# Performance work log

Hardware: AMD Instinct MI355X
Metric: run time of the kernel (lower is better)

The kernel has to match this reference:

```python
import jax, jax.numpy as jnp
import numpy as np
from jax import lax

B_J0 = 0.01      # baseline threshold b_j0
BETA = 1.8       # adaptation strength (isAdapt=1)
GAMMA = 0.5      # surrogate-gradient scale
LENS = 0.5       # surrogate-gradient window
TAU_M = 20.0     # membrane time constant
DT = 1.0
HID = 800
OUT = 10
IN = 28
DECODE = 50

@jax.custom_vjp
def act_fun(x):
    # Heaviside spike with rectangular surrogate gradient
    return (x > 0).astype(x.dtype)

def _act_fwd(x):
    return act_fun(x), x

def _act_bwd(x, g):
    return (GAMMA * g * (jnp.abs(x) < LENS).astype(g.dtype),)

act_fun.defvjp(_act_fwd, _act_bwd)

def setup_inputs() -> dict:
    key = jax.random.key(0)
    ks = jax.random.split(key, 8)
    N = 2048
    x = jax.random.normal(ks[0], (N, 784), jnp.float32)
    # xavier-ish init for i2h / h2o, orthogonal-ish scale for h2h
    W_i2h = jax.random.normal(ks[1], (HID, IN), jnp.float32) * (1.0 / np.sqrt(IN))
    b_i2h = jnp.zeros((HID,), jnp.float32)
    W_h2h = jax.random.normal(ks[2], (HID, HID), jnp.float32) * (1.0 / np.sqrt(HID))
    b_h2h = jnp.zeros((HID,), jnp.float32)
    W_h2o = jax.random.normal(ks[3], (OUT, HID), jnp.float32) * (1.0 / np.sqrt(HID))
    b_h2o = jax.random.normal(ks[4], (OUT,), jnp.float32) * 0.01
    tau_adp_h = jnp.full((HID,), 700.0, jnp.float32)
    tau_adp_o = jnp.full((OUT,), 700.0, jnp.float32)
    return {"x": x, "W_i2h": W_i2h, "b_i2h": b_i2h, "W_h2h": W_h2h,
            "b_h2h": b_h2h, "W_h2o": W_h2o, "b_h2o": b_h2o,
            "tau_adp_h": tau_adp_h, "tau_adp_o": tau_adp_o}

def reference(x, W_i2h, b_i2h, W_h2h, b_h2h, W_h2o, b_h2o, tau_adp_h, tau_adp_o):
    N = x.shape[0]
    T = 784 // IN  # 28 encode steps
    # [N, 784] -> [N, IN, T] -> pad 50 zero decode steps -> time-major [T+50, N, IN]
    seq = x.reshape(N, IN, T)
    seq = jnp.concatenate([seq, jnp.zeros((N, IN, DECODE), seq.dtype)], axis=2)
    seq = jnp.transpose(seq, (2, 0, 1))
    alpha = jnp.exp(-DT / jnp.asarray(TAU_M, x.dtype))
    ro_h = jnp.exp(-DT / tau_adp_h)  # [HID]
    ro_o = jnp.exp(-DT / tau_adp_o)  # [OUT]
    mask = (jnp.arange(T + DECODE) >= T).astype(x.dtype)  # accumulate only decode steps

    def step(carry, inp):
        h_mem, h_spk, b_h, o_mem, o_spk, b_o, acc = carry
        xt, m = inp
        # hidden adaptive-LIF update (mem_update_NU_adp)
        h_in = xt @ W_i2h.T + b_i2h + h_spk @ W_h2h.T + b_h2h
        b_h = ro_h * b_h + (1.0 - ro_h) * h_spk
        Bh = B_J0 + BETA * b_h
        h_mem = h_mem * alpha + (1.0 - alpha) * h_in - Bh * h_spk * DT
        h_spk = act_fun(h_mem - Bh)
        # output adaptive-LIF update (mem_update_adp with h2o)
        o_in = h_spk @ W_h2o.T + b_h2o
        b_o = ro_o * b_o + (1.0 - ro_o) * o_spk
        Bo = B_J0 + BETA * b_o
        o_mem = o_mem * alpha + (1.0 - alpha) * o_in - Bo * o_spk * DT
        o_spk = act_fun(o_mem - Bo)
        acc = acc + m * o_spk
        return (h_mem, h_spk, b_h, o_mem, o_spk, b_o, acc), None

    carry0 = (jnp.zeros((N, HID), x.dtype), jnp.zeros((N, HID), x.dtype),
              jnp.full((N, HID), B_J0, x.dtype),
              jnp.zeros((N, OUT), x.dtype), jnp.zeros((N, OUT), x.dtype),
              jnp.full((N, OUT), B_J0, x.dtype),
              jnp.zeros((N, OUT), x.dtype))
    final, _ = lax.scan(step, carry0, (seq, mask))
    return final[6]
```

## Files before the change

### kernel.cpp

```cpp
#include <hip/hip_runtime.h>
#include <math.h>
#include <stdint.h>

namespace {
constexpr int N_    = 2048;
constexpr int H_    = 800;
constexpr int IN_   = 28;
constexpr int TENC  = 28;
constexpr int TTOT  = 78;
constexpr int ONUM  = 10;
constexpr int PODS  = 8;
constexpr int PBLK  = 26;
constexpr int NBLK  = PODS * PBLK;
constexpr int NTILE = 26;
constexpr int FSTR  = 32;
constexpr int NSEG  = 13 * 4 * 2;
constexpr int SMEM_B = NSEG * 1024;
constexpr int SMEM_W = IN_ * 32 * 4;
constexpr int AROW  = 27;
constexpr int SMEM_A = 8 * 32 * AROW * 4;
constexpr int SMEM_TOT = SMEM_B + SMEM_W + SMEM_A;
}

typedef __attribute__((ext_vector_type(4))) int v4i;

__device__ __forceinline__ void digitize(float w, int8_t d[4]) {
    double dd = (double)w * 4294967296.0;
    long long r = (long long)rint(dd);
    int8_t d0 = (int8_t)(r & 255); r = (r - (long long)d0) >> 8;
    int8_t d1 = (int8_t)(r & 255); r = (r - (long long)d1) >> 8;
    int8_t d2 = (int8_t)(r & 255); r = (r - (long long)d2) >> 8;
    long long r3 = r; r3 = r3 > 127 ? 127 : (r3 < -128 ? -128 : r3);
    d[0] = d0; d[1] = d1; d[2] = d2; d[3] = (int8_t)r3;
}

__device__ __forceinline__ v4i unpack16(uint32_t u) {
    v4i f;
    f[0] = (int)((((u      ) & 0xFu) * 0x00204081u) & 0x01010101u);
    f[1] = (int)((((u >>  4) & 0xFu) * 0x00204081u) & 0x01010101u);
    f[2] = (int)((((u >>  8) & 0xFu) * 0x00204081u) & 0x01010101u);
    f[3] = (int)((((u >> 12) & 0xFu) * 0x00204081u) & 0x01010101u);
    return f;
}

__device__ __forceinline__ void pod_barrier(uint32_t* __restrict__ flags,
                                            int pod, int l, uint32_t epoch) {
    __syncthreads();
    if (threadIdx.x < 64) {
        if (threadIdx.x == 0) {
            asm volatile("s_waitcnt vmcnt(0)" ::: "memory");
            __hip_atomic_store(flags + pod * FSTR + l, epoch,
                               __ATOMIC_RELAXED, __HIP_MEMORY_SCOPE_AGENT);
        }
        const bool mine = (threadIdx.x < PBLK);
        bool done = false;
        while (!done) {
            bool ok = true;
            if (mine)
                ok = (__hip_atomic_load(flags + pod * FSTR + threadIdx.x,
                        __ATOMIC_RELAXED, __HIP_MEMORY_SCOPE_AGENT) >= epoch);
            done = (__ballot(ok) == ~0ull);
            if (!done) __builtin_amdgcn_s_sleep(1);
        }
    }
    __syncthreads();
}

__global__ void prep_kernel(const float* __restrict__ x, float* __restrict__ xt2,
                            uint32_t* __restrict__ sp0, uint32_t* __restrict__ sp1,
                            uint32_t* __restrict__ flags)
{
    size_t idx = (size_t)blockIdx.x * blockDim.x + threadIdx.x;
    size_t stride = (size_t)gridDim.x * blockDim.x;
    const size_t TOT = (size_t)TENC * N_ * IN_;
    for (size_t e = idx; e < TOT; e += stride) {
        int t = (int)(e / (N_ * IN_));
        int rem = (int)(e % (N_ * IN_));
        int n = rem / IN_, c = rem % IN_;
        xt2[e] = x[(size_t)n * 784 + c * TENC + t];
    }
    const size_t PW = (size_t)NTILE * N_;
    for (size_t e = idx; e < PW; e += stride) { sp0[e] = 0u; sp1[e] = 0u; }
    for (size_t e = idx; e < (size_t)PODS * FSTR; e += stride) flags[e] = 0u;
}

__global__ __launch_bounds__(512)
__attribute__((amdgpu_waves_per_eu(2)))
void lsnn_persist(const float* __restrict__ xt2,
                  const float* __restrict__ Wi,
                  const float* __restrict__ b_i2h,
                  const float* __restrict__ Wh,
                  const float* __restrict__ b_h2h,
                  const float* __restrict__ Wo,
                  const float* __restrict__ b_h2o,
                  const float* __restrict__ tau_h,
                  const float* __restrict__ tau_o,
                  uint32_t* sp0, uint32_t* sp1,
                  uint32_t* flags,
                  float* __restrict__ out)
{
    extern __shared__ __align__(16) int8_t smem[];
    int8_t*   Bl  = smem;
    float*    wl  = (float*)(smem + SMEM_B);
    uint32_t* Alds = (uint32_t*)(smem + SMEM_B + SMEM_W);

    const int bid  = blockIdx.x;
    const int pod  = bid / PBLK;
    const int l    = bid % PBLK;
    const bool is_o = (l == 25);
    const int it   = is_o ? 0 : l;
    const int i0   = it * 32;
    const int wv   = threadIdx.x >> 6;
    const int lane = threadIdx.x & 63;
    const int quad = lane >> 4;
    const int col  = lane & 15;
    const int n0   = pod * 256 + wv * 32;
    uint32_t* ldsA = Alds + wv * 32 * AROW;
    const int dsel = (quad >> 1);
    const int dsh  = (quad & 1) * 16;

    for (int e = threadIdx.x; e < 13 * 2 * 64; e += 512) {
        int c  = e >> 7;
        int bh = (e >> 6) & 1;
        int ln = e & 63;
        int q  = ln >> 4, cl = ln & 15;
        int kbase = c * 64 + q * 16;
        uint32_t w4[4][4] = {};
        int row = bh * 16 + cl;
        #pragma unroll
        for (int j = 0; j < 16; ++j) {
            int kidx = kbase + j;
            float w = 0.f;
            if (kidx < H_) {
                if (!is_o) w = Wh[(size_t)(i0 + row) * H_ + kidx];
                else if (bh == 0 && cl < ONUM) w = Wo[(size_t)cl * H_ + kidx];
            }
            int8_t d[4]; digitize(w, d);
            #pragma unroll
            for (int k = 0; k < 4; ++k)
                w4[k][j >> 2] |= ((uint32_t)(uint8_t)d[k]) << ((j & 3) * 8);
        }
        #pragma unroll
        for (int k = 0; k < 4; ++k) {
            v4i v; v[0] = (int)w4[k][0]; v[1] = (int)w4[k][1];
            v[2] = (int)w4[k][2]; v[3] = (int)w4[k][3];
            *(v4i*)(Bl + (((c * 8) + k * 2 + bh) << 10) + (ln << 4)) = v;
        }
    }
    if (!is_o) {
        for (int e = threadIdx.x; e < IN_ * 32; e += 512) {
            int c = e >> 5, il = e & 31;
            wl[c * 32 + il] = Wi[(size_t)(i0 + il) * IN_ + c];
        }
    }

    const float alpha = (float)exp((double)(-1.0f / 20.0f));
    const float onem  = 1.0f - alpha;
    const double INV32 = 1.0 / 4294967296.0;

    float roB[2] = {}, biB[2] = {}, bhB[2] = {};
    float hm[2][2][4] = {}, hbv[2][2][4];
    float om[2][4] = {}, ospv[2][4] = {}, obb[2][4], cnt[2][4] = {};
    float roO = 0.f, boO = 0.f;
    uint32_t pmask = 0;

    if (!is_o) {
        #pragma unroll
        for (int b = 0; b < 2; ++b) {
            int i = i0 + b * 16 + col;
            float arg = -1.0f / tau_h[i];
            roB[b] = (float)exp((double)arg);
            biB[b] = b_i2h[i]; bhB[b] = b_h2h[i];
        }
        #pragma unroll
        for (int a = 0; a < 2; ++a)
            #pragma unroll
            for (int b = 0; b < 2; ++b)
                #pragma unroll
                for (int r = 0; r < 4; ++r) hbv[a][b][r] = 0.01f;
    } else {
        if (col < ONUM) {
            float arg = -1.0f / tau_o[col];
            roO = (float)exp((double)arg);
            boO = b_h2o[col];
        }
        #pragma unroll
        for (int a = 0; a < 2; ++a)
            #pragma unroll
            for (int r = 0; r < 4; ++r) obb[a][r] = 0.01f;
    }

    uint32_t goff[13]; int loffv[13];
    #pragma unroll
    for (int k = 0; k < 13; ++k) {
        int tile = 2 * k + (lane >> 5);
        goff[k]  = (uint32_t)(tile * N_ + n0 + (lane & 31));
        loffv[k] = (lane & 31) * AROW + tile;
    }
    const int jrow = lane & 31;
    const int src  = ((jrow >> 2) & 3) * 16 + ((jrow >> 4) << 2) + (jrow & 3);

    __syncthreads();
    uint32_t epoch = 1;

    for (int t = 0; t <= TTOT; ++t) {
        const uint32_t* rdP = (t & 1) ? sp1 : sp0;
        uint32_t*       wrP = (t & 1) ? sp0 : sp1;

        const bool active = is_o ? (t >= 1) : (t < TTOT);

        if (active) {
            #pragma unroll
            for (int k = 0; k < 13; ++k) {
                uint32_t v = __hip_atomic_load(rdP + goff[k],
                        __ATOMIC_RELAXED, __HIP_MEMORY_SCOPE_AGENT);
                ldsA[loffv[k]] = v;
            }
        }

        if (!is_o && active) {
            float inpf[2][2][4] = {};
            if (t < TENC) {
                #pragma unroll
                for (int a = 0; a < 2; ++a) {
                    #pragma unroll
                    for (int r = 0; r < 4; ++r) {
                        int n = n0 + a * 16 + quad * 4 + r;
                        const float* xp = xt2 + ((size_t)t * N_ + n) * IN_;
                        double s0 = 0.0, s1 = 0.0;
                        #pragma unroll
                        for (int c = 0; c < IN_; ++c) {
                            double xv = (double)xp[c];
                            s0 += xv * (double)wl[c * 32 + col];
                            s1 += xv * (double)wl[c * 32 + 16 + col];
                        }
                        inpf[a][0][r] = (float)s0;
                        inpf[a][1][r] = (float)s1;
                    }
                }
            }

            v4i acc4[2][2][4] = {};
            #pragma unroll
            for (int c = 0; c < 13; ++c) {
                uint32_t d0 = ldsA[col * AROW + c * 2 + dsel];
                uint32_t d1 = ldsA[(16 + col) * AROW + c * 2 + dsel];
                v4i a0 = unpack16((d0 >> dsh) & 0xFFFFu);
                v4i a1 = unpack16((d1 >> dsh) & 0xFFFFu);
                #pragma unroll
                for (int k = 0; k < 4; ++k) {
                    v4i b0 = *(const v4i*)(Bl + (((c * 8) + k * 2 + 0) << 10) + (lane << 4));
                    v4i b1 = *(const v4i*)(Bl + (((c * 8) + k * 2 + 1) << 10) + (lane << 4));
                    acc4[0][0][k] = __builtin_amdgcn_mfma_i32_16x16x64_i8(a0, b0, acc4[0][0][k], 0, 0, 0);
                    acc4[0][1][k] = __builtin_amdgcn_mfma_i32_16x16x64_i8(a0, b1, acc4[0][1][k], 0, 0, 0);
                    acc4[1][0][k] = __builtin_amdgcn_mfma_i32_16x16x64_i8(a1, b0, acc4[1][0][k], 0, 0, 0);
                    acc4[1][1][k] = __builtin_amdgcn_mfma_i32_16x16x64_i8(a1, b1, acc4[1][1][k], 0, 0, 0);
                }
            }

            uint32_t nmask = 0;
            {
                #pragma clang fp contract(off)
                #pragma unroll
                for (int a = 0; a < 2; ++a) {
                    #pragma unroll
                    for (int b = 0; b < 2; ++b) {
                        #pragma unroll
                        for (int r = 0; r < 4; ++r) {
                            int sidx = ((a * 2 + b) * 4 + r);
                            int64_t tot = ((int64_t)acc4[a][b][3][r] << 24)
                                        + ((int64_t)acc4[a][b][2][r] << 16)
                                        + ((int64_t)acc4[a][b][1][r] << 8)
                                        +  (int64_t)acc4[a][b][0][r];
                            float rec = (float)((double)tot * INV32);
                            float h_in = ((inpf[a][b][r] + biB[b]) + rec) + bhB[b];
                            float sp = (pmask >> sidx) & 1u ? 1.0f : 0.0f;
                            float ro = roB[b];
                            float bnew = (ro * hbv[a][b][r]) + ((1.0f - ro) * sp);
                            float B = 0.01f + (1.8f * bnew);
                            float mem = ((hm[a][b][r] * alpha) + (onem * h_in)) - (B * sp);
                            float s = (mem - B) > 0.f ? 1.f : 0.f;
                            hbv[a][b][r] = bnew; hm[a][b][r] = mem;
                            if (s > 0.5f) nmask |= (1u << sidx);
                        }
                    }
                }
            }
            pmask = nmask;

            uint32_t wmine = 0;
            #pragma unroll
            for (int a = 0; a < 2; ++a) {
                #pragma unroll
                for (int r = 0; r < 4; ++r) {
                    unsigned long long bal0 = __ballot((nmask >> (a * 8 + r)) & 1u);
                    unsigned long long bal1 = __ballot((nmask >> (a * 8 + 4 + r)) & 1u);
                    if (col == a * 4 + r) {
                        wmine = (uint32_t)((bal0 >> (quad * 16)) & 0xFFFFull)
                              | ((uint32_t)((bal1 >> (quad * 16)) & 0xFFFFull) << 16);
                    }
                }
            }
            {
                uint32_t myw = (uint32_t)__shfl((int)wmine, src, 64);
                if (lane < 32)
                    __hip_atomic_store(wrP + (size_t)it * N_ + n0 + jrow, myw,
                                       __ATOMIC_RELAXED, __HIP_MEMORY_SCOPE_AGENT);
            }
        }

        if (is_o && active) {
            v4i oacc[2][4] = {};
            #pragma unroll
            for (int c = 0; c < 13; ++c) {
                uint32_t d0 = ldsA[col * AROW + c * 2 + dsel];
                uint32_t d1 = ldsA[(16 + col) * AROW + c * 2 + dsel];
                v4i a0 = unpack16((d0 >> dsh) & 0xFFFFu);
                v4i a1 = unpack16((d1 >> dsh) & 0xFFFFu);
                #pragma unroll
                for (int k = 0; k < 4; ++k) {
                    v4i bo = *(const v4i*)(Bl + (((c * 8) + k * 2 + 0) << 10) + (lane << 4));
                    oacc[0][k] = __builtin_amdgcn_mfma_i32_16x16x64_i8(a0, bo, oacc[0][k], 0, 0, 0);
                    oacc[1][k] = __builtin_amdgcn_mfma_i32_16x16x64_i8(a1, bo, oacc[1][k], 0, 0, 0);
                }
            }
            if (col < ONUM) {
                #pragma clang fp contract(off)
                const bool msk = (t - 1) >= TENC;
                #pragma unroll
                for (int a = 0; a < 2; ++a) {
                    #pragma unroll
                    for (int r = 0; r < 4; ++r) {
                        int64_t tot = ((int64_t)oacc[a][3][r] << 24)
                                    + ((int64_t)oacc[a][2][r] << 16)
                                    + ((int64_t)oacc[a][1][r] << 8)
                                    +  (int64_t)oacc[a][0][r];
                        float o_in = ((float)((double)tot * INV32)) + boO;
                        float osp_ = ospv[a][r];
                        float bnew = (roO * obb[a][r]) + ((1.0f - roO) * osp_);
                        float B = 0.01f + (1.8f * bnew);
                        float mem = ((om[a][r] * alpha) + (onem * o_in)) - (B * osp_);
                        float s = (mem - B) > 0.f ? 1.f : 0.f;
                        obb[a][r] = bnew; om[a][r] = mem; ospv[a][r] = s;
                        if (msk) cnt[a][r] += s;
                    }
                }
            }
        }

        if (t < TTOT) pod_barrier(flags, pod, l, epoch++);
    }

    if (is_o && col < ONUM) {
        #pragma unroll
        for (int a = 0; a < 2; ++a)
            #pragma unroll
            for (int r = 0; r < 4; ++r) {
                int n = n0 + a * 16 + quad * 4 + r;
                out[(size_t)n * ONUM + col] = cnt[a][r];
            }
    }
}

extern "C" void kernel_launch(void* const* d_in, const int* in_sizes, int n_in,
                              void* d_out, int out_size, void* d_ws, size_t ws_size,
                              hipStream_t stream)
{
    const float* x      = (const float*)d_in[0];
    const float* Wi     = (const float*)d_in[1];
    const float* b_i2h  = (const float*)d_in[2];
    const float* Wh     = (const float*)d_in[3];
    const float* b_h2h  = (const float*)d_in[4];
    const float* Wo     = (const float*)d_in[5];
    const float* b_h2o  = (const float*)d_in[6];
    const float* tau_h  = (const float*)d_in[7];
    const float* tau_o  = (const float*)d_in[8];
    float* out = (float*)d_out;

    uintptr_t p = (uintptr_t)d_ws;
    auto alloc = [&](size_t bytes) -> void* {
        p = (p + 255) & ~(uintptr_t)255;
        void* r = (void*)p; p += bytes; return r;
    };
    uint32_t* sp0   = (uint32_t*)alloc((size_t)NTILE * N_ * 4);
    uint32_t* sp1   = (uint32_t*)alloc((size_t)NTILE * N_ * 4);
    float*    xt2   = (float*)alloc((size_t)TENC * N_ * IN_ * 4);
    uint32_t* flags = (uint32_t*)alloc((size_t)PODS * FSTR * 4);

    prep_kernel<<<1024, 256, 0, stream>>>(x, xt2, sp0, sp1, flags);

    (void)hipFuncSetAttribute((const void*)lsnn_persist,
                              hipFuncAttributeMaxDynamicSharedMemorySize, SMEM_TOT);
    lsnn_persist<<<NBLK, 512, SMEM_TOT, stream>>>(
        xt2, Wi, b_i2h, Wh, b_h2h, Wo, b_h2o, tau_h, tau_o,
        sp0, sp1, flags, out);
}
```

Before: 1.386 ms.

## Replace per-step pod barrier with per-wave flag signaling between producers and consumers

Removes the block-wide pod barrier, which needed two __syncthreads plus a spin on every block's flag, and gives each wave its own flag row per pod. Each wave publishes a step counter after writing its spike tile, or after reading for output waves. Consumers spin only on the flags of the matching wave slots before loading. This turns a global lockstep barrier into finer-grained point-to-point dependencies, so waves can run ahead independently. In exchange it adds more flag traffic, and it risks races if the read-after-write ordering on the double buffer is not fully covered, since the output wave writes slot 25, which may alias a hidden block's slot.

```diff
diff --git a/kernel.cpp b/kernel.cpp
--- a/kernel.cpp
+++ b/kernel.cpp
@@ -43,29 +43,6 @@
     return f;
 }
 
-__device__ __forceinline__ void pod_barrier(uint32_t* __restrict__ flags,
-                                            int pod, int l, uint32_t epoch) {
-    __syncthreads();
-    if (threadIdx.x < 64) {
-        if (threadIdx.x == 0) {
-            asm volatile("s_waitcnt vmcnt(0)" ::: "memory");
-            __hip_atomic_store(flags + pod * FSTR + l, epoch,
-                               __ATOMIC_RELAXED, __HIP_MEMORY_SCOPE_AGENT);
-        }
-        const bool mine = (threadIdx.x < PBLK);
-        bool done = false;
-        while (!done) {
-            bool ok = true;
-            if (mine)
-                ok = (__hip_atomic_load(flags + pod * FSTR + threadIdx.x,
-                        __ATOMIC_RELAXED, __HIP_MEMORY_SCOPE_AGENT) >= epoch);
-            done = (__ballot(ok) == ~0ull);
-            if (!done) __builtin_amdgcn_s_sleep(1);
-        }
-    }
-    __syncthreads();
-}
-
 __global__ void prep_kernel(const float* __restrict__ x, float* __restrict__ xt2,
                             uint32_t* __restrict__ sp0, uint32_t* __restrict__ sp1,
                             uint32_t* __restrict__ flags)
@@ -81,7 +58,7 @@
     }
     const size_t PW = (size_t)NTILE * N_;
     for (size_t e = idx; e < PW; e += stride) { sp0[e] = 0u; sp1[e] = 0u; }
-    for (size_t e = idx; e < (size_t)PODS * FSTR; e += stride) flags[e] = 0u;
+    for (size_t e = idx; e < (size_t)PODS * 8 * FSTR; e += stride) flags[e] = 0u;
 }
 
 __global__ __launch_bounds__(512)
@@ -200,14 +177,29 @@
     const int jrow = lane & 31;
     const int src  = ((jrow >> 2) & 3) * 16 + ((jrow >> 4) << 2) + (jrow & 3);
 
+    uint32_t* flrow = flags + ((size_t)(pod * 8 + wv)) * FSTR;
+    const int myslot = is_o ? 25 : l;
+    const int pslot  = (lane < PBLK) ? lane : 0;
+    const bool pmine = (lane < PBLK);
+
     __syncthreads();
-    uint32_t epoch = 1;
 
     for (int t = 0; t <= TTOT; ++t) {
         const uint32_t* rdP = (t & 1) ? sp1 : sp0;
         uint32_t*       wrP = (t & 1) ? sp0 : sp1;
 
         const bool active = is_o ? (t >= 1) : (t < TTOT);
+
+        if (active && t > 0) {
+            while (true) {
+                uint32_t fv = __hip_atomic_load(flrow + pslot,
+                        __ATOMIC_RELAXED, __HIP_MEMORY_SCOPE_AGENT);
+                bool ok = !pmine || (fv >= (uint32_t)t);
+                if (__ballot(ok) == ~0ull) break;
+                __builtin_amdgcn_s_sleep(1);
+            }
+            __builtin_amdgcn_sched_barrier(0);
+        }
 
         if (active) {
             #pragma unroll
@@ -216,6 +208,13 @@
                         __ATOMIC_RELAXED, __HIP_MEMORY_SCOPE_AGENT);
                 ldsA[loffv[k]] = v;
             }
+        }
+
+        if (is_o) {
+            asm volatile("s_waitcnt vmcnt(0)" ::: "memory");
+            if (lane == 0)
+                __hip_atomic_store(flrow + myslot, (uint32_t)(t + 1),
+                                   __ATOMIC_RELAXED, __HIP_MEMORY_SCOPE_AGENT);
         }
 
         if (!is_o && active) {
@@ -307,6 +306,10 @@
                     __hip_atomic_store(wrP + (size_t)it * N_ + n0 + jrow, myw,
                                        __ATOMIC_RELAXED, __HIP_MEMORY_SCOPE_AGENT);
             }
+            asm volatile("s_waitcnt vmcnt(0)" ::: "memory");
+            if (lane == 0)
+                __hip_atomic_store(flrow + myslot, (uint32_t)(t + 1),
+                                   __ATOMIC_RELAXED, __HIP_MEMORY_SCOPE_AGENT);
         }
 
         if (is_o && active) {
@@ -347,8 +350,6 @@
                 }
             }
         }
-
-        if (t < TTOT) pod_barrier(flags, pod, l, epoch++);
     }
 
     if (is_o && col < ONUM) {
@@ -385,7 +386,7 @@
     uint32_t* sp0   = (uint32_t*)alloc((size_t)NTILE * N_ * 4);
     uint32_t* sp1   = (uint32_t*)alloc((size_t)NTILE * N_ * 4);
     float*    xt2   = (float*)alloc((size_t)TENC * N_ * IN_ * 4);
-    uint32_t* flags = (uint32_t*)alloc((size_t)PODS * FSTR * 4);
+    uint32_t* flags = (uint32_t*)alloc((size_t)PODS * 8 * FSTR * 4);
 
     prep_kernel<<<1024, 256, 0, stream>>>(x, xt2, sp0, sp1, flags);
 
```

After: 1.413 ms. Within noise of the previous version (+1.9%).

## Overlap spike-state loads with input projection, skip padded tile, widen stores

Applied to the files above, without the earlier changes.

Loads the previous step's spike words into registers first, then computes the double-precision input projection, then writes the loaded words to shared memory, so global load latency overlaps arithmetic. The always-empty 26th tile is no longer loaded; its LDS slot is zeroed once at start instead. Spike words are now published as 64-bit atomic stores from 16 lanes instead of 32-bit stores from 32 lanes. The pod barrier spin switches to a longer sleep after a few polls, which cuts polling traffic but can add wake-up latency.

```diff
diff --git a/kernel.cpp b/kernel.cpp
--- a/kernel.cpp
+++ b/kernel.cpp
@@ -54,13 +54,18 @@
         }
         const bool mine = (threadIdx.x < PBLK);
         bool done = false;
+        int itc = 0;
         while (!done) {
             bool ok = true;
             if (mine)
                 ok = (__hip_atomic_load(flags + pod * FSTR + threadIdx.x,
                         __ATOMIC_RELAXED, __HIP_MEMORY_SCOPE_AGENT) >= epoch);
             done = (__ballot(ok) == ~0ull);
-            if (!done) __builtin_amdgcn_s_sleep(1);
+            if (!done) {
+                if (itc < 4) __builtin_amdgcn_s_sleep(1);
+                else         __builtin_amdgcn_s_sleep(8);
+                ++itc;
+            }
         }
     }
     __syncthreads();
@@ -153,6 +158,7 @@
             wl[c * 32 + il] = Wi[(size_t)(i0 + il) * IN_ + c];
         }
     }
+    if (lane >= 32) ldsA[(lane & 31) * AROW + 25] = 0u;
 
     const float alpha = (float)exp((double)(-1.0f / 20.0f));
     const float onem  = 1.0f - alpha;
@@ -197,8 +203,10 @@
         goff[k]  = (uint32_t)(tile * N_ + n0 + (lane & 31));
         loffv[k] = (lane & 31) * AROW + tile;
     }
-    const int jrow = lane & 31;
-    const int src  = ((jrow >> 2) & 3) * 16 + ((jrow >> 4) << 2) + (jrow & 3);
+    const int j0 = (lane & 15) * 2;
+    const int j1 = j0 + 1;
+    const int s0 = ((j0 >> 2) & 3) * 16 + ((j0 >> 4) << 2) + (j0 & 3);
+    const int s1 = ((j1 >> 2) & 3) * 16 + ((j1 >> 4) << 2) + (j1 & 3);
 
     __syncthreads();
     uint32_t epoch = 1;
@@ -209,37 +217,46 @@
 
         const bool active = is_o ? (t >= 1) : (t < TTOT);
 
+        uint32_t vv[13];
         if (active) {
             #pragma unroll
             for (int k = 0; k < 13; ++k) {
-                uint32_t v = __hip_atomic_load(rdP + goff[k],
-                        __ATOMIC_RELAXED, __HIP_MEMORY_SCOPE_AGENT);
-                ldsA[loffv[k]] = v;
+                const bool real = (k < 12) || (lane < 32);
+                vv[k] = real ? __hip_atomic_load(rdP + goff[k],
+                            __ATOMIC_RELAXED, __HIP_MEMORY_SCOPE_AGENT) : 0u;
+            }
+        }
+
+        float inpf[2][2][4] = {};
+        if (!is_o && active && t < TENC) {
+            #pragma unroll
+            for (int a = 0; a < 2; ++a) {
+                #pragma unroll
+                for (int r = 0; r < 4; ++r) {
+                    int n = n0 + a * 16 + quad * 4 + r;
+                    const float* xp = xt2 + ((size_t)t * N_ + n) * IN_;
+                    double s0d = 0.0, s1d = 0.0;
+                    #pragma unroll
+                    for (int c = 0; c < IN_; ++c) {
+                        double xv = (double)xp[c];
+                        s0d += xv * (double)wl[c * 32 + col];
+                        s1d += xv * (double)wl[c * 32 + 16 + col];
+                    }
+                    inpf[a][0][r] = (float)s0d;
+                    inpf[a][1][r] = (float)s1d;
+                }
+            }
+        }
+
+        if (active) {
+            #pragma unroll
+            for (int k = 0; k < 13; ++k) {
+                const bool real = (k < 12) || (lane < 32);
+                if (real) ldsA[loffv[k]] = vv[k];
             }
         }
 
         if (!is_o && active) {
-            float inpf[2][2][4] = {};
-            if (t < TENC) {
-                #pragma unroll
-                for (int a = 0; a < 2; ++a) {
-                    #pragma unroll
-                    for (int r = 0; r < 4; ++r) {
-                        int n = n0 + a * 16 + quad * 4 + r;
-                        const float* xp = xt2 + ((size_t)t * N_ + n) * IN_;
-                        double s0 = 0.0, s1 = 0.0;
-                        #pragma unroll
-                        for (int c = 0; c < IN_; ++c) {
-                            double xv = (double)xp[c];
-                            s0 += xv * (double)wl[c * 32 + col];
-                            s1 += xv * (double)wl[c * 32 + 16 + col];
-                        }
-                        inpf[a][0][r] = (float)s0;
-                        inpf[a][1][r] = (float)s1;
-                    }
-                }
-            }
-
             v4i acc4[2][2][4] = {};
             #pragma unroll
             for (int c = 0; c < 13; ++c) {
@@ -302,10 +319,14 @@
                 }
             }
             {
-                uint32_t myw = (uint32_t)__shfl((int)wmine, src, 64);
-                if (lane < 32)
-                    __hip_atomic_store(wrP + (size_t)it * N_ + n0 + jrow, myw,
+                uint32_t g0 = (uint32_t)__shfl((int)wmine, s0, 64);
+                uint32_t g1 = (uint32_t)__shfl((int)wmine, s1, 64);
+                if (lane < 16) {
+                    uint64_t q = (uint64_t)g0 | ((uint64_t)g1 << 32);
+                    uint64_t* qp = (uint64_t*)(wrP + (size_t)it * N_ + n0);
+                    __hip_atomic_store(qp + (lane & 15), q,
                                        __ATOMIC_RELAXED, __HIP_MEMORY_SCOPE_AGENT);
+                }
             }
         }
 
```

Result: no change. 1.383 ms (-0.2%).
